# Optimization experiments

Hardware: AMD Instinct MI355X
Metric: run time of the kernel (lower is better)

## Reference

```python
import jax, jax.numpy as jnp
import numpy as np

VOCAB, EMBED, EN_H, DE_H, ATTN, LAYERS = 50000, 256, 512, 512, 256, 2
SEQ, BATCH = 1024, 64

def setup_inputs() -> dict:
    key = jax.random.key(0)
    ks = jax.random.split(key, 20)
    n = lambda k, shp: jax.random.normal(k, shp, dtype=jnp.float32)
    inp = {
        "cur_input": jax.random.randint(ks[0], (BATCH,), 0, VOCAB, dtype=jnp.int64) if jax.config.jax_enable_x64 else jax.random.randint(ks[0], (BATCH,), 0, VOCAB, dtype=jnp.int32),
        "h0": n(ks[1], (LAYERS, BATCH, DE_H)),
        "c0": n(ks[2], (LAYERS, BATCH, DE_H)),
        "enc_states": n(ks[3], (SEQ, BATCH, EN_H)),
        "attention_mask": jnp.ones((BATCH, SEQ), dtype=jnp.float32),
        # parameters
        "emb_table": n(ks[4], (VOCAB, EMBED)) * 0.02,
        "attn_W": n(ks[5], (EN_H + DE_H, ATTN)) * 0.02,   # attention_model: Linear(en+de, attn, bias=False)
        "attn_v": n(ks[6], (ATTN,)) * 0.02,               # Linear(attn, 1, bias=False)
        "cg_W": n(ks[7], (DE_H + EMBED + EN_H, EN_H)) * 0.02,  # context gate
        "cg_b": jnp.zeros((EN_H,), dtype=jnp.float32),
        "Wih0": n(ks[8], (4 * DE_H, EN_H + EMBED)) * 0.02,
        "Whh0": n(ks[9], (4 * DE_H, DE_H)) * 0.02,
        "bih0": jnp.zeros((4 * DE_H,), dtype=jnp.float32),
        "bhh0": jnp.zeros((4 * DE_H,), dtype=jnp.float32),
        "Wih1": n(ks[10], (4 * DE_H, DE_H)) * 0.02,
        "Whh1": n(ks[11], (4 * DE_H, DE_H)) * 0.02,
        "bih1": jnp.zeros((4 * DE_H,), dtype=jnp.float32),
        "bhh1": jnp.zeros((4 * DE_H,), dtype=jnp.float32),
        "out_W": n(ks[12], (DE_H, VOCAB)) * 0.02,
        "out_b": jnp.zeros((VOCAB,), dtype=jnp.float32),
    }
    return inp

def _lstm_cell(x, h, c, Wih, Whh, bih, bhh):
    gates = x @ Wih.T + h @ Whh.T + bih + bhh  # (B, 4H), torch gate order i,f,g,o
    i, f, g, o = jnp.split(gates, 4, axis=-1)
    c_new = jax.nn.sigmoid(f) * c + jax.nn.sigmoid(i) * jnp.tanh(g)
    h_new = jax.nn.sigmoid(o) * jnp.tanh(c_new)
    return h_new, c_new

def reference(cur_input, h0, c0, enc_states, attention_mask,
              emb_table, attn_W, attn_v, cg_W, cg_b,
              Wih0, Whh0, bih0, bhh0, Wih1, Whh1, bih1, bhh1,
              out_W, out_b):
    S, B, _ = enc_states.shape
    dec = h0[-1]  # (B, DE_H)
    # Bahdanau attention: score over seq dim
    dec_b = jnp.broadcast_to(dec[None], (S, B, dec.shape[-1]))
    feat = jnp.tanh(jnp.concatenate([enc_states, dec_b], axis=-1) @ attn_W)  # (S,B,ATTN)
    e = feat @ attn_v  # (S,B)
    e = jnp.where(attention_mask.T > 0, e, jnp.float32(-1e9))
    alpha = jax.nn.softmax(e, axis=0)  # (S,B)
    ctx = jnp.einsum('sb,sbh->bh', alpha, enc_states)  # (B, EN_H)
    # embedding + context gate
    emb = emb_table[cur_input]  # (B, EMBED)
    gate = jax.nn.sigmoid(jnp.concatenate([dec, emb, ctx], axis=-1) @ cg_W + cg_b)
    ctx = gate * ctx
    x = jnp.concatenate([emb, ctx], axis=-1)  # (B, EMBED+EN_H)
    # two-layer single-step LSTM
    h1, c1 = _lstm_cell(x, h0[0], c0[0], Wih0, Whh0, bih0, bhh0)
    h2, c2 = _lstm_cell(h1, h0[1], c0[1], Wih1, Whh1, bih1, bhh1)
    out = h2 @ out_W + out_b  # (B, VOCAB)
    return out, jnp.stack([h1, h2]), jnp.stack([c1, c2])
```

## Files before the change

### kernel.cpp

```cpp
#include <hip/hip_runtime.h>
#include <math.h>


typedef __attribute__((ext_vector_type(8))) short short8;
typedef __attribute__((ext_vector_type(4))) float f32x4;

__device__ __forceinline__ float sigf(float x) { return 1.f / (1.f + expf(-x)); }

__device__ __forceinline__ unsigned short f2bf(float f) {
    unsigned int u = __builtin_bit_cast(unsigned int, f);
    unsigned int r = (u + 0x7fffu + ((u >> 16) & 1u)) >> 16;
    return (unsigned short)r;
}

__device__ __forceinline__ float tanh_fast(float x) {
    float t = __expf(2.f * x);
    return 1.f - 2.f * __builtin_amdgcn_rcpf(1.f + t);
}

__global__ void k_convW(const float* __restrict__ W, unsigned short* __restrict__ Wt) {
    __shared__ float tile[64][65];
    int kb = blockIdx.x * 64, nb = blockIdx.y * 64;
    int t = threadIdx.x;
    int r0 = t >> 6, c = t & 63;
#pragma unroll
    for (int i = 0; i < 16; ++i) {
        int r = i * 4 + r0;
        tile[r][c] = W[(size_t)(kb + r) * 256 + nb + c];
    }
    __syncthreads();
#pragma unroll
    for (int i = 0; i < 16; ++i) {
        int r = i * 4 + r0;
        Wt[(size_t)(nb + r) * 512 + kb + c] = f2bf(tile[c][r]);
    }
}

__global__ void k_prep(const int* __restrict__ cur, const float* __restrict__ h0,
                       const float* __restrict__ emb_table, const float* __restrict__ attn_W,
                       float* __restrict__ X1, float* __restrict__ X2, float* __restrict__ X3,
                       float* __restrict__ decW) {
    int b = blockIdx.x, t = threadIdx.x;
    __shared__ float dec_s[512];
    const float* dec = h0 + (size_t)(64 + b) * 512;
    for (int i = t; i < 512; i += 256) {
        float v = dec[i];
        dec_s[i] = v;
        X1[b * 1280 + i] = v;
        X2[b * 1280 + 768 + i] = h0[(size_t)b * 512 + i];
        X3[b * 1024 + 512 + i] = v;
    }
    int row = cur[b];
    float ev = emb_table[(size_t)row * 256 + t];
    X1[b * 1280 + 512 + t] = ev;
    X2[b * 1280 + t] = ev;
    __syncthreads();
    float acc = 0.f;
    for (int k = 0; k < 512; ++k)
        acc += dec_s[k] * attn_W[(size_t)(512 + k) * 256 + t];
    decW[b * 256 + t] = acc;
}

__global__ __launch_bounds__(256) void k_scores_mfma(
        const float* __restrict__ enc, const unsigned short* __restrict__ Wt,
        const float* __restrict__ attn_v, const float* __restrict__ decW,
        float* __restrict__ e_out) {
    int s = blockIdx.x, t = threadIdx.x;
    __shared__ __align__(16) unsigned short sA[4096];
    __shared__ __align__(16) unsigned short sB[16384];
    const float* arow = enc + (size_t)s * 64 * 512;
    int w = t >> 6, l = t & 63, li = l & 15, lg = l >> 4;
    int sw = (li & 7) << 4;

    f32x4 acc[4][4];
#pragma unroll
    for (int rt = 0; rt < 4; ++rt)
#pragma unroll
        for (int ct = 0; ct < 4; ++ct) acc[rt][ct] = (f32x4){0.f, 0.f, 0.f, 0.f};

    for (int kk = 0; kk < 512; kk += 64) {
        __syncthreads();
#pragma unroll
        for (int i = 0; i < 2; ++i) {
            int idx = i * 256 + t, row = idx >> 3, kg = idx & 7;
            const float* g = arow + row * 512 + kk + kg * 8;
            float4 p0 = *(const float4*)g;
            float4 p1 = *(const float4*)(g + 4);
            uint4 wv;
            wv.x = f2bf(p0.x) | ((unsigned)f2bf(p0.y) << 16);
            wv.y = f2bf(p0.z) | ((unsigned)f2bf(p0.w) << 16);
            wv.z = f2bf(p1.x) | ((unsigned)f2bf(p1.y) << 16);
            wv.w = f2bf(p1.z) | ((unsigned)f2bf(p1.w) << 16);
            int byte = (row * 128 + kg * 16) ^ ((row & 7) << 4);
            *(uint4*)((char*)sA + byte) = wv;
        }
#pragma unroll
        for (int i = 0; i < 8; ++i) {
            int idx = i * 256 + t, n = idx >> 3, kg = idx & 7;
            uint4 wv = *(const uint4*)(Wt + (size_t)n * 512 + kk + kg * 8);
            int byte = (n * 128 + kg * 16) ^ ((n & 7) << 4);
            *(uint4*)((char*)sB + byte) = wv;
        }
        __syncthreads();
#pragma unroll
        for (int ks = 0; ks < 2; ++ks) {
            short8 af[4], bf[4];
#pragma unroll
            for (int rt = 0; rt < 4; ++rt) {
                int row = rt * 16 + li;
                af[rt] = *(short8*)((char*)sA + ((row * 128 + ks * 64 + lg * 16) ^ sw));
            }
#pragma unroll
            for (int ct = 0; ct < 4; ++ct) {
                int n = w * 64 + ct * 16 + li;
                bf[ct] = *(short8*)((char*)sB + ((n * 128 + ks * 64 + lg * 16) ^ sw));
            }
#pragma unroll
            for (int rt = 0; rt < 4; ++rt)
#pragma unroll
                for (int ct = 0; ct < 4; ++ct)
                    acc[rt][ct] = __builtin_amdgcn_mfma_f32_16x16x32_bf16(
                        af[rt], bf[ct], acc[rt][ct], 0, 0, 0);
        }
    }
    float er[4][4];
#pragma unroll
    for (int rt = 0; rt < 4; ++rt)
#pragma unroll
        for (int r = 0; r < 4; ++r) er[rt][r] = 0.f;
#pragma unroll
    for (int ct = 0; ct < 4; ++ct) {
        int a = w * 64 + ct * 16 + li;
        float v = attn_v[a];
#pragma unroll
        for (int rt = 0; rt < 4; ++rt) {
#pragma unroll
            for (int r = 0; r < 4; ++r) {
                int row = rt * 16 + lg * 4 + r;
                float x = acc[rt][ct][r] + decW[row * 256 + a];
                er[rt][r] += tanh_fast(x) * v;
            }
        }
    }
#pragma unroll
    for (int off = 1; off < 16; off <<= 1)
#pragma unroll
        for (int rt = 0; rt < 4; ++rt)
#pragma unroll
            for (int r = 0; r < 4; ++r)
                er[rt][r] += __shfl_xor(er[rt][r], off, 64);
    __syncthreads();
    float* part = (float*)sA;
    if (li == 0) {
#pragma unroll
        for (int rt = 0; rt < 4; ++rt)
#pragma unroll
            for (int r = 0; r < 4; ++r)
                part[w * 64 + rt * 16 + lg * 4 + r] = er[rt][r];
    }
    __syncthreads();
    if (t < 64)
        e_out[t * 1024 + s] = part[t] + part[64 + t] + part[128 + t] + part[192 + t];
}

__global__ void k_softmax(float* __restrict__ ebuf, const float* __restrict__ mask) {
    int b = blockIdx.x, t = threadIdx.x;
    __shared__ float red[8];
    float v[4];
    float lmax = -1e30f;
#pragma unroll
    for (int si = 0; si < 4; ++si) {
        int s = si * 256 + t;
        float x = ebuf[b * 1024 + s];
        x = (mask[b * 1024 + s] > 0.f) ? x : -1e9f;
        v[si] = x; lmax = fmaxf(lmax, x);
    }
#pragma unroll
    for (int off = 32; off > 0; off >>= 1) lmax = fmaxf(lmax, __shfl_xor(lmax, off, 64));
    if ((t & 63) == 0) red[t >> 6] = lmax;
    __syncthreads();
    float m = fmaxf(fmaxf(red[0], red[1]), fmaxf(red[2], red[3]));
    float e4[4], lsum = 0.f;
#pragma unroll
    for (int si = 0; si < 4; ++si) { e4[si] = __expf(v[si] - m); lsum += e4[si]; }
#pragma unroll
    for (int off = 32; off > 0; off >>= 1) lsum += __shfl_xor(lsum, off, 64);
    if ((t & 63) == 0) red[4 + (t >> 6)] = lsum;
    __syncthreads();
    float inv = 1.f / (red[4] + red[5] + red[6] + red[7]);
#pragma unroll
    for (int si = 0; si < 4; ++si)
        ebuf[b * 1024 + si * 256 + t] = e4[si] * inv;
}

__global__ __launch_bounds__(512) void k_ctx_partial(const float* __restrict__ alpha,
        const float* __restrict__ enc, float* __restrict__ ctxP) {
    int b = blockIdx.x & 63, sc = blockIdx.x >> 6;
    int t = threadIdx.x;
    __shared__ float al[128];
    if (t < 128) al[t] = alpha[b * 1024 + sc * 128 + t];
    __syncthreads();
    const float* base = enc + (((size_t)sc * 128 * 64) + b) * 512 + t;
    float a0 = 0.f, a1 = 0.f, a2 = 0.f, a3 = 0.f;
    for (int s = 0; s < 128; s += 4) {
        float x0 = base[(size_t)(s + 0) * 32768];
        float x1 = base[(size_t)(s + 1) * 32768];
        float x2 = base[(size_t)(s + 2) * 32768];
        float x3 = base[(size_t)(s + 3) * 32768];
        a0 += al[s] * x0; a1 += al[s + 1] * x1; a2 += al[s + 2] * x2; a3 += al[s + 3] * x3;
    }
    ctxP[((size_t)sc * 64 + b) * 512 + t] = a0 + a1 + a2 + a3;
}

__global__ void k_ctx_reduce(const float* __restrict__ ctxP, float* __restrict__ X1) {
    int idx = blockIdx.x * 256 + threadIdx.x;
    int b = idx >> 9, h = idx & 511;
    float s = 0.f;
#pragma unroll
    for (int sc = 0; sc < 8; ++sc) s += ctxP[((size_t)sc * 64 + b) * 512 + h];
    X1[b * 1280 + 768 + h] = s;
}

__global__ __launch_bounds__(1024) void k_gemm_cg(const float* __restrict__ X,
        const float* __restrict__ Wkn, float* __restrict__ P) {
    int n0 = blockIdx.x * 64, sp = blockIdx.y;
    int t = threadIdx.x, tc = t & 63, tr = t >> 6;
    __shared__ __align__(16) float As[64 * 68];
    __shared__ __align__(16) float Wc[64 * 68];
    float acc[4] = {0.f, 0.f, 0.f, 0.f};
    for (int c = 0; c < 5; ++c) {
        int k0 = sp * 320 + c * 64;
        __syncthreads();
#pragma unroll
        for (int i = 0; i < 4; ++i) {
            int idx = i * 1024 + t; int row = idx >> 6; int k = idx & 63;
            As[k * 68 + row] = X[row * 1280 + k0 + k];
        }
#pragma unroll
        for (int i = 0; i < 4; ++i) {
            int idx = i * 1024 + t; int k = idx >> 6; int cc = idx & 63;
            Wc[k * 68 + cc] = Wkn[(size_t)(k0 + k) * 512 + n0 + cc];
        }
        __syncthreads();
#pragma unroll 8
        for (int k = 0; k < 64; ++k) {
            float4 a = *(const float4*)&As[k * 68 + 4 * tr];
            float wv = Wc[k * 68 + tc];
            acc[0] += a.x * wv; acc[1] += a.y * wv; acc[2] += a.z * wv; acc[3] += a.w * wv;
        }
    }
    float* Pp = P + (size_t)sp * 64 * 512;
#pragma unroll
    for (int j = 0; j < 4; ++j) Pp[(4 * tr + j) * 512 + n0 + tc] = acc[j];
}

__global__ __launch_bounds__(1024) void k_gemm_lstm(const float* __restrict__ X, int ldx,
        const float* __restrict__ W1, int K1, const float* __restrict__ W2, int K2,
        int kchunks, float* __restrict__ P) {
    int n0 = blockIdx.x * 64, sp = blockIdx.y;
    int t = threadIdx.x, tc = t & 63, tr = t >> 6;
    __shared__ __align__(16) float As[64 * 68];
    __shared__ __align__(16) float Wc[64 * 68];
    float acc[4] = {0.f, 0.f, 0.f, 0.f};
    for (int c = 0; c < kchunks; ++c) {
        int k0 = (sp * kchunks + c) * 64;
        __syncthreads();
#pragma unroll
        for (int i = 0; i < 4; ++i) {
            int idx = i * 1024 + t; int row = idx >> 6; int k = idx & 63;
            As[k * 68 + row] = X[row * ldx + k0 + k];
        }
#pragma unroll
        for (int i = 0; i < 4; ++i) {
            int idx = i * 1024 + t; int cc = idx >> 6; int k = idx & 63;
            int gk = k0 + k; int j = n0 + cc;
            float wv = (gk < K1) ? W1[(size_t)j * K1 + gk] : W2[(size_t)j * K2 + gk - K1];
            Wc[k * 68 + cc] = wv;
        }
        __syncthreads();
#pragma unroll 8
        for (int k = 0; k < 64; ++k) {
            float4 a = *(const float4*)&As[k * 68 + 4 * tr];
            float wv = Wc[k * 68 + tc];
            acc[0] += a.x * wv; acc[1] += a.y * wv; acc[2] += a.z * wv; acc[3] += a.w * wv;
        }
    }
    float* Pp = P + (size_t)sp * 64 * 2048;
#pragma unroll
    for (int j = 0; j < 4; ++j) Pp[(4 * tr + j) * 2048 + n0 + tc] = acc[j];
}

__global__ void k_cg_fin(const float* __restrict__ P, const float* __restrict__ cg_b,
                         const float* __restrict__ X1, float* __restrict__ X2) {
    int idx = blockIdx.x * 256 + threadIdx.x;
    int b = idx >> 9, h = idx & 511;
    float g = cg_b[h];
#pragma unroll
    for (int sp = 0; sp < 4; ++sp) g += P[sp * 32768 + idx];
    float gate = sigf(g);
    X2[b * 1280 + 256 + h] = gate * X1[b * 1280 + 768 + h];
}

__global__ void k_lstm_fin(const float* __restrict__ P, const float* __restrict__ bih,
                           const float* __restrict__ bhh, const float* __restrict__ c0,
                           int layer, float* __restrict__ oh, float* __restrict__ oc,
                           float* __restrict__ X3out) {
    int idx = blockIdx.x * 256 + threadIdx.x;
    int b = idx >> 9, h = idx & 511;
    float gi = bih[h] + bhh[h];
    float gf = bih[512 + h] + bhh[512 + h];
    float gg = bih[1024 + h] + bhh[1024 + h];
    float go = bih[1536 + h] + bhh[1536 + h];
#pragma unroll
    for (int sp = 0; sp < 4; ++sp) {
        const float* Pp = P + sp * 131072 + b * 2048;
        gi += Pp[h]; gf += Pp[512 + h]; gg += Pp[1024 + h]; go += Pp[1536 + h];
    }
    float cp = c0[layer * 32768 + b * 512 + h];
    float cn = sigf(gf) * cp + sigf(gi) * tanhf(gg);
    float hn = sigf(go) * tanhf(cn);
    oh[b * 512 + h] = hn;
    oc[b * 512 + h] = cn;
    if (X3out) X3out[b * 1024 + h] = hn;
}

__global__ __launch_bounds__(256) void k_outproj_mfma(
        const float* __restrict__ h2, const float* __restrict__ out_W,
        const float* __restrict__ out_b, float* __restrict__ out) {
    int t = threadIdx.x;
    int n0 = blockIdx.x * 128;
    int w = t >> 6, l = t & 63, li = l & 15, lg = l >> 4;
    int sw = (li & 7) << 4;
    __shared__ __align__(16) unsigned short sA[4096];

    f32x4 acc[4][2];
#pragma unroll
    for (int rt = 0; rt < 4; ++rt)
#pragma unroll
        for (int ct = 0; ct < 2; ++ct) acc[rt][ct] = (f32x4){0.f, 0.f, 0.f, 0.f};
    int colbase = n0 + w * 32;

    for (int kk = 0; kk < 512; kk += 64) {
        __syncthreads();
#pragma unroll
        for (int i = 0; i < 2; ++i) {
            int idx = i * 256 + t, row = idx >> 3, kg = idx & 7;
            const float* g = h2 + row * 512 + kk + kg * 8;
            float4 p0 = *(const float4*)g;
            float4 p1 = *(const float4*)(g + 4);
            uint4 wv;
            wv.x = f2bf(p0.x) | ((unsigned)f2bf(p0.y) << 16);
            wv.y = f2bf(p0.z) | ((unsigned)f2bf(p0.w) << 16);
            wv.z = f2bf(p1.x) | ((unsigned)f2bf(p1.y) << 16);
            wv.w = f2bf(p1.z) | ((unsigned)f2bf(p1.w) << 16);
            int byte = (row * 128 + kg * 16) ^ ((row & 7) << 4);
            *(uint4*)((char*)sA + byte) = wv;
        }
        __syncthreads();
#pragma unroll
        for (int ks = 0; ks < 2; ++ks) {
            short8 bf[2];
#pragma unroll
            for (int ct = 0; ct < 2; ++ct) {
                int col = colbase + ct * 16 + li;
                col = (col < 50000) ? col : 49999;
                const float* wp = out_W + (size_t)(kk + ks * 32 + lg * 8) * 50000 + col;
                uint4 qv;
                float v0 = wp[0],          v1 = wp[50000];
                float v2 = wp[2 * 50000],  v3 = wp[3 * 50000];
                float v4 = wp[4 * 50000],  v5 = wp[5 * 50000];
                float v6 = wp[6 * 50000],  v7 = wp[7 * 50000];
                qv.x = f2bf(v0) | ((unsigned)f2bf(v1) << 16);
                qv.y = f2bf(v2) | ((unsigned)f2bf(v3) << 16);
                qv.z = f2bf(v4) | ((unsigned)f2bf(v5) << 16);
                qv.w = f2bf(v6) | ((unsigned)f2bf(v7) << 16);
                bf[ct] = *(short8*)&qv;
            }
            short8 af[4];
#pragma unroll
            for (int rt = 0; rt < 4; ++rt) {
                int row = rt * 16 + li;
                af[rt] = *(short8*)((char*)sA + ((row * 128 + ks * 64 + lg * 16) ^ sw));
            }
#pragma unroll
            for (int rt = 0; rt < 4; ++rt)
#pragma unroll
                for (int ct = 0; ct < 2; ++ct)
                    acc[rt][ct] = __builtin_amdgcn_mfma_f32_16x16x32_bf16(
                        af[rt], bf[ct], acc[rt][ct], 0, 0, 0);
        }
    }
#pragma unroll
    for (int ct = 0; ct < 2; ++ct) {
        int col = colbase + ct * 16 + li;
        if (col < 50000) {
            float bias = out_b[col];
#pragma unroll
            for (int rt = 0; rt < 4; ++rt)
#pragma unroll
                for (int r = 0; r < 4; ++r) {
                    int row = rt * 16 + lg * 4 + r;
                    out[(size_t)row * 50000 + col] = acc[rt][ct][r] + bias;
                }
        }
    }
}

extern "C" void kernel_launch(void* const* d_in, const int* in_sizes, int n_in,
                              void* d_out, int out_size, void* d_ws, size_t ws_size,
                              hipStream_t stream) {
    const int*   cur       = (const int*)d_in[0];
    const float* h0        = (const float*)d_in[1];
    const float* c0        = (const float*)d_in[2];
    const float* enc       = (const float*)d_in[3];
    const float* mask      = (const float*)d_in[4];
    const float* emb_table = (const float*)d_in[5];
    const float* attn_W    = (const float*)d_in[6];
    const float* attn_v    = (const float*)d_in[7];
    const float* cg_W      = (const float*)d_in[8];
    const float* cg_b      = (const float*)d_in[9];
    const float* Wih0      = (const float*)d_in[10];
    const float* Whh0      = (const float*)d_in[11];
    const float* bih0      = (const float*)d_in[12];
    const float* bhh0      = (const float*)d_in[13];
    const float* Wih1      = (const float*)d_in[14];
    const float* Whh1      = (const float*)d_in[15];
    const float* bih1      = (const float*)d_in[16];
    const float* bhh1      = (const float*)d_in[17];
    const float* out_W     = (const float*)d_in[18];
    const float* out_b     = (const float*)d_in[19];
    float* out = (float*)d_out;

    float* w    = (float*)d_ws;
    float* X1   = w;
    float* X2   = X1 + 81920;
    float* X3   = X2 + 81920;
    float* decW = X3 + 65536;
    float* eb   = decW + 16384;
    float* P    = eb + 65536;
    unsigned short* Wt = (unsigned short*)P;
    float* ctxP = P + 65536;

    float* outH = out + 3200000;
    float* outC = out + 3265536;

    hipLaunchKernelGGL(k_convW, dim3(8, 4), dim3(256), 0, stream, attn_W, Wt);
    hipLaunchKernelGGL(k_prep, dim3(64), dim3(256), 0, stream,
                       cur, h0, emb_table, attn_W, X1, X2, X3, decW);
    hipLaunchKernelGGL(k_scores_mfma, dim3(1024), dim3(256), 0, stream,
                       enc, Wt, attn_v, decW, eb);
    hipLaunchKernelGGL(k_softmax, dim3(64), dim3(256), 0, stream, eb, mask);
    hipLaunchKernelGGL(k_ctx_partial, dim3(512), dim3(512), 0, stream, eb, enc, ctxP);
    hipLaunchKernelGGL(k_ctx_reduce, dim3(128), dim3(256), 0, stream, ctxP, X1);
    hipLaunchKernelGGL(k_gemm_cg, dim3(8, 4), dim3(1024), 0, stream, X1, cg_W, P);
    hipLaunchKernelGGL(k_cg_fin, dim3(128), dim3(256), 0, stream, P, cg_b, X1, X2);
    hipLaunchKernelGGL(k_gemm_lstm, dim3(32, 4), dim3(1024), 0, stream,
                       X2, 1280, Wih0, 768, Whh0, 512, 5, P);
    hipLaunchKernelGGL(k_lstm_fin, dim3(128), dim3(256), 0, stream,
                       P, bih0, bhh0, c0, 0, outH, outC, X3);
    hipLaunchKernelGGL(k_gemm_lstm, dim3(32, 4), dim3(1024), 0, stream,
                       X3, 1024, Wih1, 512, Whh1, 512, 4, P);
    hipLaunchKernelGGL(k_lstm_fin, dim3(128), dim3(256), 0, stream,
                       P, bih1, bhh1, c0, 1, outH + 32768, outC + 32768, (float*)nullptr);
    hipLaunchKernelGGL(k_outproj_mfma, dim3(391), dim3(256), 0, stream,
                       outH + 32768, out_W, out_b, out);
}
```

Before: 187.6 us.

## Load MFMA operands directly from global memory, dropping LDS staging

The attention score kernel no longer stages the encoder tile and the bf16 weight tile through shared memory with barriers. Each wave now loads its own MFMA fragments straight from global memory (converting encoder rows to bf16 in registers) and issues MFMAs without synchronisation. This removes LDS traffic and __syncthreads, but each of the four waves now reloads the same encoder fragments independently. The global accesses are also less coalesced: each lane reads 32 bytes at a 2KB row stride.

Result: slower. 247.9 us (+32.1%).

```diff
diff --git a/kernel.cpp b/kernel.cpp
--- a/kernel.cpp
+++ b/kernel.cpp
@@ -66,11 +66,9 @@
         const float* __restrict__ attn_v, const float* __restrict__ decW,
         float* __restrict__ e_out) {
     int s = blockIdx.x, t = threadIdx.x;
-    __shared__ __align__(16) unsigned short sA[4096];
-    __shared__ __align__(16) unsigned short sB[16384];
+    int w = t >> 6, l = t & 63, li = l & 15, lg = l >> 4;
     const float* arow = enc + (size_t)s * 64 * 512;
-    int w = t >> 6, l = t & 63, li = l & 15, lg = l >> 4;
-    int sw = (li & 7) << 4;
+    __shared__ float part[256];
 
     f32x4 acc[4][4];
 #pragma unroll
@@ -78,12 +76,12 @@
 #pragma unroll
         for (int ct = 0; ct < 4; ++ct) acc[rt][ct] = (f32x4){0.f, 0.f, 0.f, 0.f};
 
-    for (int kk = 0; kk < 512; kk += 64) {
-        __syncthreads();
-#pragma unroll
-        for (int i = 0; i < 2; ++i) {
-            int idx = i * 256 + t, row = idx >> 3, kg = idx & 7;
-            const float* g = arow + row * 512 + kk + kg * 8;
+#pragma unroll 2
+    for (int kk = 0; kk < 512; kk += 32) {
+        short8 af[4], bf[4];
+#pragma unroll
+        for (int rt = 0; rt < 4; ++rt) {
+            const float* g = arow + (rt * 16 + li) * 512 + kk + lg * 8;
             float4 p0 = *(const float4*)g;
             float4 p1 = *(const float4*)(g + 4);
             uint4 wv;
@@ -91,38 +89,19 @@
             wv.y = f2bf(p0.z) | ((unsigned)f2bf(p0.w) << 16);
             wv.z = f2bf(p1.x) | ((unsigned)f2bf(p1.y) << 16);
             wv.w = f2bf(p1.z) | ((unsigned)f2bf(p1.w) << 16);
-            int byte = (row * 128 + kg * 16) ^ ((row & 7) << 4);
-            *(uint4*)((char*)sA + byte) = wv;
-        }
-#pragma unroll
-        for (int i = 0; i < 8; ++i) {
-            int idx = i * 256 + t, n = idx >> 3, kg = idx & 7;
-            uint4 wv = *(const uint4*)(Wt + (size_t)n * 512 + kk + kg * 8);
-            int byte = (n * 128 + kg * 16) ^ ((n & 7) << 4);
-            *(uint4*)((char*)sB + byte) = wv;
-        }
-        __syncthreads();
-#pragma unroll
-        for (int ks = 0; ks < 2; ++ks) {
-            short8 af[4], bf[4];
-#pragma unroll
-            for (int rt = 0; rt < 4; ++rt) {
-                int row = rt * 16 + li;
-                af[rt] = *(short8*)((char*)sA + ((row * 128 + ks * 64 + lg * 16) ^ sw));
-            }
-#pragma unroll
-            for (int ct = 0; ct < 4; ++ct) {
-                int n = w * 64 + ct * 16 + li;
-                bf[ct] = *(short8*)((char*)sB + ((n * 128 + ks * 64 + lg * 16) ^ sw));
-            }
-#pragma unroll
-            for (int rt = 0; rt < 4; ++rt)
-#pragma unroll
-                for (int ct = 0; ct < 4; ++ct)
-                    acc[rt][ct] = __builtin_amdgcn_mfma_f32_16x16x32_bf16(
-                        af[rt], bf[ct], acc[rt][ct], 0, 0, 0);
-        }
-    }
+            af[rt] = __builtin_bit_cast(short8, wv);
+        }
+#pragma unroll
+        for (int ct = 0; ct < 4; ++ct)
+            bf[ct] = *(const short8*)(Wt + (size_t)(w * 64 + ct * 16 + li) * 512 + kk + lg * 8);
+#pragma unroll
+        for (int rt = 0; rt < 4; ++rt)
+#pragma unroll
+            for (int ct = 0; ct < 4; ++ct)
+                acc[rt][ct] = __builtin_amdgcn_mfma_f32_16x16x32_bf16(
+                    af[rt], bf[ct], acc[rt][ct], 0, 0, 0);
+    }
+
     float er[4][4];
 #pragma unroll
     for (int rt = 0; rt < 4; ++rt)
@@ -149,8 +128,6 @@
 #pragma unroll
             for (int r = 0; r < 4; ++r)
                 er[rt][r] += __shfl_xor(er[rt][r], off, 64);
-    __syncthreads();
-    float* part = (float*)sA;
     if (li == 0) {
 #pragma unroll
         for (int rt = 0; rt < 4; ++rt)
```

## Fuse softmax into ctx partial, fold ctx reduce into consumers, merge prep kernels

Applied to the files above, without the earlier changes.

Merges the weight-conversion and prep kernels into one launch by assigning extra blocks to the transpose. The softmax is recomputed redundantly inside each ctx_partial block rather than run as a separate kernel, and the ctx partial-sum reduction is folded into the context-gate GEMM A-tile load and into cg_fin. This removes three kernel launches and their global round-trips, at the cost of each ctx block rereading all 1024 scores and the GEMM redoing the 8-way reduction per tile. The ctxP buffer is moved further into the workspace so it does not overlap P.

New measurement: 187.7 us. Within noise of the previous version (+0.1%).

```diff
diff --git a/kernel.cpp b/kernel.cpp
--- a/kernel.cpp
+++ b/kernel.cpp
@@ -18,30 +18,31 @@
     return 1.f - 2.f * __builtin_amdgcn_rcpf(1.f + t);
 }
 
-__global__ void k_convW(const float* __restrict__ W, unsigned short* __restrict__ Wt) {
-    __shared__ float tile[64][65];
-    int kb = blockIdx.x * 64, nb = blockIdx.y * 64;
+__global__ void k_prep_conv(const int* __restrict__ cur, const float* __restrict__ h0,
+                            const float* __restrict__ emb_table, const float* __restrict__ attn_W,
+                            float* __restrict__ X1, float* __restrict__ X2, float* __restrict__ X3,
+                            float* __restrict__ decW, unsigned short* __restrict__ Wt) {
     int t = threadIdx.x;
-    int r0 = t >> 6, c = t & 63;
-#pragma unroll
-    for (int i = 0; i < 16; ++i) {
-        int r = i * 4 + r0;
-        tile[r][c] = W[(size_t)(kb + r) * 256 + nb + c];
-    }
-    __syncthreads();
-#pragma unroll
-    for (int i = 0; i < 16; ++i) {
-        int r = i * 4 + r0;
-        Wt[(size_t)(nb + r) * 512 + kb + c] = f2bf(tile[c][r]);
-    }
-}
-
-__global__ void k_prep(const int* __restrict__ cur, const float* __restrict__ h0,
-                       const float* __restrict__ emb_table, const float* __restrict__ attn_W,
-                       float* __restrict__ X1, float* __restrict__ X2, float* __restrict__ X3,
-                       float* __restrict__ decW) {
-    int b = blockIdx.x, t = threadIdx.x;
+    if (blockIdx.x >= 64) {
+        __shared__ float tile[64][65];
+        int bx = blockIdx.x - 64;
+        int kb = (bx & 7) * 64, nb = (bx >> 3) * 64;
+        int r0 = t >> 6, c = t & 63;
+#pragma unroll
+        for (int i = 0; i < 16; ++i) {
+            int r = i * 4 + r0;
+            tile[r][c] = attn_W[(size_t)(kb + r) * 256 + nb + c];
+        }
+        __syncthreads();
+#pragma unroll
+        for (int i = 0; i < 16; ++i) {
+            int r = i * 4 + r0;
+            Wt[(size_t)(nb + r) * 512 + kb + c] = f2bf(tile[c][r]);
+        }
+        return;
+    }
     __shared__ float dec_s[512];
+    int b = blockIdx.x;
     const float* dec = h0 + (size_t)(64 + b) * 512;
     for (int i = t; i < 512; i += 256) {
         float v = dec[i];
@@ -163,42 +164,40 @@
         e_out[t * 1024 + s] = part[t] + part[64 + t] + part[128 + t] + part[192 + t];
 }
 
-__global__ void k_softmax(float* __restrict__ ebuf, const float* __restrict__ mask) {
-    int b = blockIdx.x, t = threadIdx.x;
-    __shared__ float red[8];
-    float v[4];
-    float lmax = -1e30f;
-#pragma unroll
-    for (int si = 0; si < 4; ++si) {
-        int s = si * 256 + t;
-        float x = ebuf[b * 1024 + s];
-        x = (mask[b * 1024 + s] > 0.f) ? x : -1e9f;
-        v[si] = x; lmax = fmaxf(lmax, x);
-    }
-#pragma unroll
-    for (int off = 32; off > 0; off >>= 1) lmax = fmaxf(lmax, __shfl_xor(lmax, off, 64));
-    if ((t & 63) == 0) red[t >> 6] = lmax;
-    __syncthreads();
-    float m = fmaxf(fmaxf(red[0], red[1]), fmaxf(red[2], red[3]));
-    float e4[4], lsum = 0.f;
-#pragma unroll
-    for (int si = 0; si < 4; ++si) { e4[si] = __expf(v[si] - m); lsum += e4[si]; }
-#pragma unroll
-    for (int off = 32; off > 0; off >>= 1) lsum += __shfl_xor(lsum, off, 64);
-    if ((t & 63) == 0) red[4 + (t >> 6)] = lsum;
-    __syncthreads();
-    float inv = 1.f / (red[4] + red[5] + red[6] + red[7]);
-#pragma unroll
-    for (int si = 0; si < 4; ++si)
-        ebuf[b * 1024 + si * 256 + t] = e4[si] * inv;
-}
-
-__global__ __launch_bounds__(512) void k_ctx_partial(const float* __restrict__ alpha,
-        const float* __restrict__ enc, float* __restrict__ ctxP) {
+__global__ __launch_bounds__(512) void k_ctx_partial(const float* __restrict__ ebuf,
+        const float* __restrict__ mask, const float* __restrict__ enc,
+        float* __restrict__ ctxP) {
     int b = blockIdx.x & 63, sc = blockIdx.x >> 6;
     int t = threadIdx.x;
     __shared__ float al[128];
-    if (t < 128) al[t] = alpha[b * 1024 + sc * 128 + t];
+    __shared__ float red[16];
+    float v0 = ebuf[b * 1024 + t];
+    float v1 = ebuf[b * 1024 + 512 + t];
+    v0 = (mask[b * 1024 + t] > 0.f) ? v0 : -1e9f;
+    v1 = (mask[b * 1024 + 512 + t] > 0.f) ? v1 : -1e9f;
+    float lmax = fmaxf(v0, v1);
+#pragma unroll
+    for (int off = 32; off > 0; off >>= 1) lmax = fmaxf(lmax, __shfl_xor(lmax, off, 64));
+    if ((t & 63) == 0) red[t >> 6] = lmax;
+    __syncthreads();
+    float m = red[0];
+#pragma unroll
+    for (int i = 1; i < 8; ++i) m = fmaxf(m, red[i]);
+    float lsum = __expf(v0 - m) + __expf(v1 - m);
+#pragma unroll
+    for (int off = 32; off > 0; off >>= 1) lsum += __shfl_xor(lsum, off, 64);
+    if ((t & 63) == 0) red[8 + (t >> 6)] = lsum;
+    __syncthreads();
+    float tot = red[8];
+#pragma unroll
+    for (int i = 1; i < 8; ++i) tot += red[8 + i];
+    float inv = 1.f / tot;
+    if (t < 128) {
+        int s = sc * 128 + t;
+        float x = ebuf[b * 1024 + s];
+        x = (mask[b * 1024 + s] > 0.f) ? x : -1e9f;
+        al[t] = __expf(x - m) * inv;
+    }
     __syncthreads();
     const float* base = enc + (((size_t)sc * 128 * 64) + b) * 512 + t;
     float a0 = 0.f, a1 = 0.f, a2 = 0.f, a3 = 0.f;
@@ -212,17 +211,9 @@
     ctxP[((size_t)sc * 64 + b) * 512 + t] = a0 + a1 + a2 + a3;
 }
 
-__global__ void k_ctx_reduce(const float* __restrict__ ctxP, float* __restrict__ X1) {
-    int idx = blockIdx.x * 256 + threadIdx.x;
-    int b = idx >> 9, h = idx & 511;
-    float s = 0.f;
-#pragma unroll
-    for (int sc = 0; sc < 8; ++sc) s += ctxP[((size_t)sc * 64 + b) * 512 + h];
-    X1[b * 1280 + 768 + h] = s;
-}
-
 __global__ __launch_bounds__(1024) void k_gemm_cg(const float* __restrict__ X,
-        const float* __restrict__ Wkn, float* __restrict__ P) {
+        const float* __restrict__ ctxP, const float* __restrict__ Wkn,
+        float* __restrict__ P) {
     int n0 = blockIdx.x * 64, sp = blockIdx.y;
     int t = threadIdx.x, tc = t & 63, tr = t >> 6;
     __shared__ __align__(16) float As[64 * 68];
@@ -234,7 +225,18 @@
 #pragma unroll
         for (int i = 0; i < 4; ++i) {
             int idx = i * 1024 + t; int row = idx >> 6; int k = idx & 63;
-            As[k * 68 + row] = X[row * 1280 + k0 + k];
+            int gk = k0 + k;
+            float v;
+            if (gk < 768) {
+                v = X[row * 1280 + gk];
+            } else {
+                int h = gk - 768;
+                v = 0.f;
+#pragma unroll
+                for (int sc = 0; sc < 8; ++sc)
+                    v += ctxP[((size_t)sc * 64 + row) * 512 + h];
+            }
+            As[k * 68 + row] = v;
         }
 #pragma unroll
         for (int i = 0; i < 4; ++i) {
@@ -291,14 +293,16 @@
 }
 
 __global__ void k_cg_fin(const float* __restrict__ P, const float* __restrict__ cg_b,
-                         const float* __restrict__ X1, float* __restrict__ X2) {
+                         const float* __restrict__ ctxP, float* __restrict__ X2) {
     int idx = blockIdx.x * 256 + threadIdx.x;
     int b = idx >> 9, h = idx & 511;
     float g = cg_b[h];
 #pragma unroll
     for (int sp = 0; sp < 4; ++sp) g += P[sp * 32768 + idx];
-    float gate = sigf(g);
-    X2[b * 1280 + 256 + h] = gate * X1[b * 1280 + 768 + h];
+    float ctx = 0.f;
+#pragma unroll
+    for (int sc = 0; sc < 8; ++sc) ctx += ctxP[((size_t)sc * 64 + b) * 512 + h];
+    X2[b * 1280 + 256 + h] = sigf(g) * ctx;
 }
 
 __global__ void k_lstm_fin(const float* __restrict__ P, const float* __restrict__ bih,
@@ -440,20 +444,20 @@
     float* P    = eb + 65536;
     unsigned short* Wt = (unsigned short*)P;
     float* ctxP = P + 65536;
+    ctxP = P + 524288;
 
     float* outH = out + 3200000;
     float* outC = out + 3265536;
 
-    hipLaunchKernelGGL(k_convW, dim3(8, 4), dim3(256), 0, stream, attn_W, Wt);
-    hipLaunchKernelGGL(k_prep, dim3(64), dim3(256), 0, stream,
-                       cur, h0, emb_table, attn_W, X1, X2, X3, decW);
+    hipLaunchKernelGGL(k_prep_conv, dim3(96), dim3(256), 0, stream,
+                       cur, h0, emb_table, attn_W, X1, X2, X3, decW, Wt);
     hipLaunchKernelGGL(k_scores_mfma, dim3(1024), dim3(256), 0, stream,
                        enc, Wt, attn_v, decW, eb);
-    hipLaunchKernelGGL(k_softmax, dim3(64), dim3(256), 0, stream, eb, mask);
-    hipLaunchKernelGGL(k_ctx_partial, dim3(512), dim3(512), 0, stream, eb, enc, ctxP);
-    hipLaunchKernelGGL(k_ctx_reduce, dim3(128), dim3(256), 0, stream, ctxP, X1);
-    hipLaunchKernelGGL(k_gemm_cg, dim3(8, 4), dim3(1024), 0, stream, X1, cg_W, P);
-    hipLaunchKernelGGL(k_cg_fin, dim3(128), dim3(256), 0, stream, P, cg_b, X1, X2);
+    hipLaunchKernelGGL(k_ctx_partial, dim3(512), dim3(512), 0, stream,
+                       eb, mask, enc, ctxP);
+    hipLaunchKernelGGL(k_gemm_cg, dim3(8, 4), dim3(1024), 0, stream,
+                       X1, ctxP, cg_W, P);
+    hipLaunchKernelGGL(k_cg_fin, dim3(128), dim3(256), 0, stream, P, cg_b, ctxP, X2);
     hipLaunchKernelGGL(k_gemm_lstm, dim3(32, 4), dim3(1024), 0, stream,
                        X2, 1280, Wih0, 768, Whh0, 512, 5, P);
     hipLaunchKernelGGL(k_lstm_fin, dim3(128), dim3(256), 0, stream,
```
